# Performance work log

Measured on AMD Instinct MI355X. Metric: run time of the kernel, lower is better.

Reference implementation:

```python
import jax, jax.numpy as jnp
import numpy as np
import math

N, E, D, H, C, G = 100000, 1600000, 256, 256, 4, 512
LN_EPS = 1e-5


def _pe(n, d):
    # sinusoidal positional encoding, rows = node index
    pos = jnp.arange(n, dtype=jnp.float32)[:, None]                      # [n,1]
    div = jnp.exp(jnp.arange(0, d, 2, dtype=jnp.float32) * (-math.log(10000.0) / d))  # [d/2]
    ang = pos * div                                                      # [n,d/2]
    return jnp.stack([jnp.sin(ang), jnp.cos(ang)], axis=-1).reshape(n, d)


def setup_inputs() -> dict:
    key = jax.random.key(0)
    ks = jax.random.split(key, 24)
    w = lambda k, shp: (jax.random.normal(k, shp, jnp.float32) * 0.05)
    inp = {
        "x": jax.random.normal(ks[0], (N, D), jnp.float32),
        "W_ft": w(ks[1], (D, H)), "b_ft": jnp.zeros((H,), jnp.float32),
        "ln_g": jnp.ones((H,), jnp.float32), "ln_b": jnp.zeros((H,), jnp.float32),
        "W_g0": w(ks[2], (H, H)), "b_g0": jnp.zeros((H,), jnp.float32),
        "W_g1": w(ks[3], (H, H)), "b_g1": jnp.zeros((H,), jnp.float32),
        "W_g2": w(ks[4], (H, H)), "b_g2": jnp.zeros((H,), jnp.float32),
        "W_c0": w(ks[5], (H, H)), "b_c0": jnp.zeros((H,), jnp.float32),
        "W_c1": w(ks[6], (H, H // 2)), "b_c1": jnp.zeros((H // 2,), jnp.float32),
        "W_c2": w(ks[7], (H // 2, C)), "b_c2": jnp.zeros((C,), jnp.float32),
        "edge_index": jax.random.randint(ks[8], (2, E), 0, N, dtype=jnp.int32),
        "batch": jnp.sort(jax.random.randint(ks[9], (N,), 0, G, dtype=jnp.int32)),
    }
    return inp


def reference(x, W_ft, b_ft, ln_g, ln_b, W_g0, b_g0, W_g1, b_g1, W_g2, b_g2,
              W_c0, b_c0, W_c1, b_c1, W_c2, b_c2, edge_index, batch):
    # feature transform: Linear + ReLU + Dropout(eval) + LayerNorm
    h = jax.nn.relu(x @ W_ft + b_ft)
    mu = jnp.mean(h, axis=-1, keepdims=True)
    var = jnp.mean(jnp.square(h - mu), axis=-1, keepdims=True)
    h = (h - mu) * jax.lax.rsqrt(var + LN_EPS) * ln_g + ln_b
    # temporal positional encoding (intended per-node add)
    h = h + _pe(N, H)
    # GCN layers (PyG GCNConv: self-loops + symmetric degree norm + scatter-add)
    loops = jnp.arange(N, dtype=edge_index.dtype)
    src = jnp.concatenate([edge_index[0], loops])
    dst = jnp.concatenate([edge_index[1], loops])
    deg = jax.ops.segment_sum(jnp.ones_like(dst, dtype=h.dtype), dst, num_segments=N)
    dinv = jnp.where(deg > 0, jax.lax.rsqrt(jnp.maximum(deg, 1.0)), 0.0)
    norm = (dinv[src] * dinv[dst])[:, None]                              # [E+N,1]
    for W, b in ((W_g0, b_g0), (W_g1, b_g1), (W_g2, b_g2)):
        m = (h @ W)[src] * norm                                          # gather + scale
        h = jax.nn.relu(jax.ops.segment_sum(m, dst, num_segments=N) + b)
    # global mean pool per graph
    sums = jax.ops.segment_sum(h, batch, num_segments=G)
    cnts = jax.ops.segment_sum(jnp.ones((N,), h.dtype), batch, num_segments=G)
    pooled = sums / jnp.maximum(cnts, 1.0)[:, None]                      # [G,H]
    # classifier MLP
    z = jax.nn.relu(pooled @ W_c0 + b_c0)
    z = jax.nn.relu(z @ W_c1 + b_c1)
    return z @ W_c2 + b_c2                                               # [G,C]
```

## Files before the change

kernel.cpp:

```cpp
#include <hip/hip_runtime.h>
#include <math.h>


typedef __attribute__((ext_vector_type(8))) _Float16 half8;
typedef __attribute__((ext_vector_type(4))) float floatx4;
typedef __attribute__((ext_vector_type(8))) unsigned short us8;

union HU { _Float16 h; unsigned short u; };

static __device__ __forceinline__ unsigned short f2h(float f) {
    HU x; x.h = (_Float16)f; return x.u;
}
static __device__ __forceinline__ float h2f(unsigned short s) {
    HU x; x.u = s; return (float)x.h;
}

static __device__ __forceinline__ void gl_lds16(const void* g, void* l) {
    __builtin_amdgcn_global_load_lds(
        (const __attribute__((address_space(1))) unsigned int*)(g),
        (__attribute__((address_space(3))) unsigned int*)(l), 16, 0, 0);
}

static __device__ __forceinline__ float cw_trig(float ang, bool is_cos) {
    const float i2pi = 0.15915494309189535f;
    const float k = rintf(ang * i2pi);
    float r = fmaf(k, -6.28125f, ang);
    r = fmaf(k, -1.9352436065673828e-3f, r);
    r = fmaf(k, -6.3573019e-8f, r);
    const float rv = r * i2pi;
    return is_cos ? __builtin_amdgcn_cosf(rv) : __builtin_amdgcn_sinf(rv);
}

__global__ void tg_splitB(const float* __restrict__ W0, const float* __restrict__ W1,
                          const float* __restrict__ W2, const float* __restrict__ W3,
                          unsigned short* __restrict__ B0, unsigned short* __restrict__ B1,
                          unsigned short* __restrict__ B2, unsigned short* __restrict__ B3)
{
    const float* Ws[4] = {W0, W1, W2, W3};
    unsigned short* Bs[4] = {B0, B1, B2, B3};
    const float* W = Ws[blockIdx.z];
    unsigned short* Bt = Bs[blockIdx.z];

    __shared__ float T[64][68];
    const int tk = blockIdx.x * 64, tn = blockIdx.y * 64;
    const int t = threadIdx.x;
#pragma unroll
    for (int j = 0; j < 4; ++j) {
        const int idx = t + 256 * j;
        const int k = idx >> 4, c4 = (idx & 15) * 4;
        const float4 v = *(const float4*)&W[(size_t)(tk + k) * 256 + tn + c4];
        T[k][c4] = v.x; T[k][c4 + 1] = v.y; T[k][c4 + 2] = v.z; T[k][c4 + 3] = v.w;
    }
    __syncthreads();
#pragma unroll
    for (int j = 0; j < 4; ++j) {
        const int idx = t + 256 * j;
        const int n = idx >> 4, q = (idx & 15) * 4;
        unsigned short hh[4], ll[4];
#pragma unroll
        for (int i = 0; i < 4; ++i) {
            const float f = T[q + i][n];
            hh[i] = f2h(f);
            ll[i] = f2h(f - h2f(hh[i]));
        }
        uint2 hp, lp;
        hp.x = (unsigned)hh[0] | ((unsigned)hh[1] << 16);
        hp.y = (unsigned)hh[2] | ((unsigned)hh[3] << 16);
        lp.x = (unsigned)ll[0] | ((unsigned)ll[1] << 16);
        lp.y = (unsigned)ll[2] | ((unsigned)ll[3] << 16);
        unsigned short* row = Bt + (size_t)(tn + n) * 512;
        *(uint2*)&row[tk + q]       = hp;
        *(uint2*)&row[256 + tk + q] = lp;
    }
}

__global__ __launch_bounds__(256, 2)
void tg_ft_ln(const float* __restrict__ x, const unsigned short* __restrict__ Bt,
              const float* __restrict__ bias, const float* __restrict__ lng,
              const float* __restrict__ lnb, unsigned short* __restrict__ hh, int N)
{
    __shared__ unsigned short sAh[128 * 64];
    __shared__ unsigned short sAl[128 * 64];
    __shared__ unsigned short sB[256 * 64];
    __shared__ float sStats[128][2][2];
    __shared__ float sDiv[128];

    const int t = threadIdx.x;
    const int w = t >> 6, lane = t & 63;
    const int quad = lane >> 4, l16 = lane & 15;
    const int wr = w >> 1, wc = w & 1;
    const int row0 = blockIdx.x * 128;

    if (t < 128) sDiv[t] = expf((float)(2 * t) * -0.035977892078031970f);

    floatx4 acc[4][8];
#pragma unroll
    for (int i = 0; i < 4; ++i)
#pragma unroll
        for (int j = 0; j < 8; ++j) acc[i][j] = (floatx4){0.f, 0.f, 0.f, 0.f};

    const int arow = t >> 1;
    const int ahalf = t & 1;
    const int srow = lane >> 3;
    const int kgx  = (lane & 7) ^ srow;
    const int rsw  = l16 & 7;

    for (int k4 = 0; k4 < 4; ++k4) {
        const int ka = k4 * 64;
        if (k4) __syncthreads();
#pragma unroll
        for (int i = 0; i < 8; ++i) {
            const int rr = w * 64 + i * 8;
            gl_lds16(Bt + (size_t)(rr + srow) * 512 + ka + kgx * 8, &sB[rr * 64]);
        }
        {
            const int grow = row0 + arow;
            const bool ok = grow < N;
            const float* xp = x + (size_t)grow * 256 + ka + ahalf * 32;
#pragma unroll
            for (int j = 0; j < 4; ++j) {
                const int kg = ahalf * 4 + j;
                float4 v0 = {0.f, 0.f, 0.f, 0.f}, v1 = {0.f, 0.f, 0.f, 0.f};
                if (ok) {
                    v0 = *(const float4*)(xp + j * 8);
                    v1 = *(const float4*)(xp + j * 8 + 4);
                }
                const float f[8] = {v0.x, v0.y, v0.z, v0.w, v1.x, v1.y, v1.z, v1.w};
                us8 hi, lo;
#pragma unroll
                for (int i = 0; i < 8; ++i) {
                    hi[i] = f2h(f[i]);
                    lo[i] = f2h(f[i] - h2f(hi[i]));
                }
                const int ad = arow * 64 + ((kg ^ (arow & 7)) << 3);
                *(us8*)&sAh[ad] = hi;
                *(us8*)&sAl[ad] = lo;
            }
        }
        __syncthreads();
#pragma unroll
        for (int ks = 0; ks < 2; ++ks) {
            const int kq = ks * 4 + quad;
            half8 afh[4], afl[4];
#pragma unroll
            for (int rt = 0; rt < 4; ++rt) {
                const int r = wr * 64 + rt * 16 + l16;
                const int off = r * 64 + ((kq ^ rsw) << 3);
                afh[rt] = *(const half8*)&sAh[off];
                afl[rt] = *(const half8*)&sAl[off];
            }
#pragma unroll
            for (int cb = 0; cb < 2; ++cb) {
                half8 bfr[4];
#pragma unroll
                for (int c4 = 0; c4 < 4; ++c4) {
                    const int n = wc * 128 + (cb * 4 + c4) * 16 + l16;
                    bfr[c4] = *(const half8*)&sB[n * 64 + ((kq ^ rsw) << 3)];
                }
#pragma unroll
                for (int c4 = 0; c4 < 4; ++c4)
#pragma unroll
                    for (int rt = 0; rt < 4; ++rt) {
                        acc[rt][cb * 4 + c4] = __builtin_amdgcn_mfma_f32_16x16x32_f16(
                            afh[rt], bfr[c4], acc[rt][cb * 4 + c4], 0, 0, 0);
                        acc[rt][cb * 4 + c4] = __builtin_amdgcn_mfma_f32_16x16x32_f16(
                            afl[rt], bfr[c4], acc[rt][cb * 4 + c4], 0, 0, 0);
                    }
            }
        }
        __syncthreads();
#pragma unroll
        for (int i = 0; i < 8; ++i) {
            const int rr = w * 64 + i * 8;
            gl_lds16(Bt + (size_t)(rr + srow) * 512 + 256 + ka + kgx * 8, &sB[rr * 64]);
        }
        __syncthreads();
#pragma unroll
        for (int ks = 0; ks < 2; ++ks) {
            const int kq = ks * 4 + quad;
            half8 afh[4];
#pragma unroll
            for (int rt = 0; rt < 4; ++rt) {
                const int r = wr * 64 + rt * 16 + l16;
                afh[rt] = *(const half8*)&sAh[r * 64 + ((kq ^ rsw) << 3)];
            }
#pragma unroll
            for (int cb = 0; cb < 2; ++cb) {
                half8 bfr[4];
#pragma unroll
                for (int c4 = 0; c4 < 4; ++c4) {
                    const int n = wc * 128 + (cb * 4 + c4) * 16 + l16;
                    bfr[c4] = *(const half8*)&sB[n * 64 + ((kq ^ rsw) << 3)];
                }
#pragma unroll
                for (int c4 = 0; c4 < 4; ++c4)
#pragma unroll
                    for (int rt = 0; rt < 4; ++rt)
                        acc[rt][cb * 4 + c4] = __builtin_amdgcn_mfma_f32_16x16x32_f16(
                            afh[rt], bfr[c4], acc[rt][cb * 4 + c4], 0, 0, 0);
            }
        }
    }

    float bs[8], gs[8], bv[8], dv[8];
#pragma unroll
    for (int ct = 0; ct < 8; ++ct) {
        const int gc = wc * 128 + ct * 16 + l16;
        bs[ct] = bias[gc]; gs[ct] = lng[gc]; bv[ct] = lnb[gc];
        dv[ct] = sDiv[gc >> 1];
    }

#pragma unroll
    for (int rt = 0; rt < 4; ++rt) {
#pragma unroll
        for (int i = 0; i < 4; ++i) {
            float s = 0.f, q = 0.f;
#pragma unroll
            for (int ct = 0; ct < 8; ++ct) {
                const float v = fmaxf(acc[rt][ct][i] + bs[ct], 0.f);
                s += v; q += v * v;
            }
#pragma unroll
            for (int m = 1; m < 16; m <<= 1) {
                s += __shfl_xor(s, m, 64);
                q += __shfl_xor(q, m, 64);
            }
            if (l16 == 0) {
                const int rl = wr * 64 + rt * 16 + quad * 4 + i;
                sStats[rl][wc][0] = s;
                sStats[rl][wc][1] = q;
            }
        }
    }
    __syncthreads();

    const bool is_cos = (l16 & 1);
#pragma unroll
    for (int rt = 0; rt < 4; ++rt) {
#pragma unroll
        for (int i = 0; i < 4; ++i) {
            const int rl = wr * 64 + rt * 16 + quad * 4 + i;
            const int gr = row0 + rl;
            if (gr >= N) continue;
            const float sum = sStats[rl][0][0] + sStats[rl][1][0];
            const float sq  = sStats[rl][0][1] + sStats[rl][1][1];
            const float mu  = sum * (1.f / 256.f);
            const float var = sq * (1.f / 256.f) - mu * mu;
            const float rstd = 1.f / sqrtf(var + 1e-5f);
            const float rf = (float)gr;
            unsigned short* orow = hh + (size_t)gr * 256 + wc * 128 + l16;
#pragma unroll
            for (int ct = 0; ct < 8; ++ct) {
                const float v = fmaxf(acc[rt][ct][i] + bs[ct], 0.f);
                const float nrm = (v - mu) * rstd * gs[ct] + bv[ct];
                const float pe = cw_trig(rf * dv[ct], is_cos);
                orow[ct * 16] = f2h(nrm + pe);
            }
        }
    }
}

__global__ __launch_bounds__(256, 3)
void tg_gemm(const unsigned short* __restrict__ Ph,
             const unsigned short* __restrict__ Bt,
             const float* __restrict__ rowscale,
             unsigned short* __restrict__ out)
{
    __shared__ unsigned short sA[128 * 64], sB[128 * 64];

    const int t = threadIdx.x;
    const int w = t >> 6, lane = t & 63;
    const int quad = lane >> 4, l16 = lane & 15;
    const int wr = w >> 1, wc = w & 1;

    const int nwg = gridDim.x;
    const int swq = nwg >> 3, swr = nwg & 7;
    const int xcd = blockIdx.x & 7, oidx = blockIdx.x >> 3;
    const int lg = (xcd < swr ? xcd * (swq + 1)
                              : swr * (swq + 1) + (xcd - swr) * swq) + oidx;
    const int row0 = (lg >> 1) * 128;
    const int col0 = (lg & 1) * 128;

    floatx4 acc[4][4];
#pragma unroll
    for (int i = 0; i < 4; ++i)
#pragma unroll
        for (int j = 0; j < 4; ++j) acc[i][j] = (floatx4){0.f, 0.f, 0.f, 0.f};

    const int srow = lane >> 3;
    const int kgx  = (lane & 7) ^ srow;
    const int rsw  = l16 & 7;

    for (int c = 0; c < 8; ++c) {
        const int ka = (c >> 1) << 6;
        const int kb = ((c & 1) << 8) + ka;
        const bool stA = !(c & 1);
        if (c) __syncthreads();
#pragma unroll
        for (int i = 0; i < 4; ++i) {
            const int rr = w * 32 + i * 8;
            if (stA)
                gl_lds16(Ph + (size_t)(row0 + rr + srow) * 256 + ka + kgx * 8, &sA[rr * 64]);
            gl_lds16(Bt + (size_t)(col0 + rr + srow) * 512 + kb + kgx * 8, &sB[rr * 64]);
        }
        __syncthreads();
#pragma unroll
        for (int ks = 0; ks < 2; ++ks) {
            const int kq = ks * 4 + quad;
            half8 af[4], bfr[4];
#pragma unroll
            for (int rt = 0; rt < 4; ++rt) {
                const int r = wr * 64 + rt * 16 + l16;
                af[rt] = *(const half8*)&sA[r * 64 + ((kq ^ rsw) << 3)];
            }
#pragma unroll
            for (int ct = 0; ct < 4; ++ct) {
                const int n = wc * 64 + ct * 16 + l16;
                bfr[ct] = *(const half8*)&sB[n * 64 + ((kq ^ rsw) << 3)];
            }
#pragma unroll
            for (int ct = 0; ct < 4; ++ct)
#pragma unroll
                for (int rt = 0; rt < 4; ++rt)
                    acc[rt][ct] = __builtin_amdgcn_mfma_f32_16x16x32_f16(
                        af[rt], bfr[ct], acc[rt][ct], 0, 0, 0);
        }
    }

#pragma unroll
    for (int rt = 0; rt < 4; ++rt) {
#pragma unroll
        for (int i = 0; i < 4; ++i) {
            const int gr = row0 + wr * 64 + rt * 16 + quad * 4 + i;
            const float s = rowscale[gr];
#pragma unroll
            for (int ct = 0; ct < 4; ++ct) {
                const int gc = col0 + wc * 64 + ct * 16 + l16;
                out[(size_t)gr * 256 + gc] = f2h(acc[rt][ct][i] * s);
            }
        }
    }
}

__global__ void tg_count(const int* __restrict__ dst, int* __restrict__ deg,
                         int* __restrict__ perm, int E)
{
    const int e = blockIdx.x * blockDim.x + threadIdx.x;
    if (e < E) perm[e] = atomicAdd(&deg[dst[e]], 1);
}

__global__ void tg_dinv(const int* __restrict__ deg, float* __restrict__ dinv, int N)
{
    const int i = blockIdx.x * blockDim.x + threadIdx.x;
    if (i < N) dinv[i] = 1.f / sqrtf((float)(deg[i] + 1));
}

__global__ void tg_scan1(const int* __restrict__ cnt, int* __restrict__ out,
                         int* __restrict__ sums, int N)
{
    __shared__ int tmp[1024];
    const int t = threadIdx.x;
    const int gid = blockIdx.x * 1024 + t;
    const int v = (gid < N) ? cnt[gid] : 0;
    tmp[t] = v;
    __syncthreads();
    for (int o = 1; o < 1024; o <<= 1) {
        const int add = (t >= o) ? tmp[t - o] : 0;
        __syncthreads();
        tmp[t] += add;
        __syncthreads();
    }
    if (gid < N) out[gid] = tmp[t] - v;
    if (t == 1023) sums[blockIdx.x] = tmp[t];
}

__global__ void tg_scan2(int* __restrict__ sums, int nb)
{
    __shared__ int tmp[1024];
    const int t = threadIdx.x;
    const int v = (t < nb) ? sums[t] : 0;
    tmp[t] = v;
    __syncthreads();
    for (int o = 1; o < 1024; o <<= 1) {
        const int add = (t >= o) ? tmp[t - o] : 0;
        __syncthreads();
        tmp[t] += add;
        __syncthreads();
    }
    if (t < nb) sums[t] = tmp[t] - v;
}

__global__ void tg_scan3(int* __restrict__ rowptr, const int* __restrict__ offs,
                         int N, int E)
{
    const int gid = blockIdx.x * 1024 + threadIdx.x;
    if (gid < N) rowptr[gid] += offs[gid >> 10];
    else if (gid == N) rowptr[N] = E;
}

__global__ void tg_fill(const int* __restrict__ src, const int* __restrict__ dst,
                        const int* __restrict__ rowptr, const int* __restrict__ perm,
                        int* __restrict__ col, int E)
{
    const int e = blockIdx.x * blockDim.x + threadIdx.x;
    if (e >= E) return;
    col[rowptr[dst[e]] + perm[e]] = src[e];
}

__global__ void tg_aggregate_h(const unsigned short* __restrict__ hwpb,
                               const int* __restrict__ rowptr, const int* __restrict__ col,
                               const float* __restrict__ dinv, const float* __restrict__ bias,
                               unsigned short* __restrict__ hh, int N)
{
    const int gt = blockIdx.x * blockDim.x + threadIdx.x;
    const int row = gt >> 5;
    if (row >= N) return;
    const int hl = gt & 31;
    const int c = hl * 8;

    const unsigned short* base = hwpb + c;
    const int beg = rowptr[row], end = rowptr[row + 1];

    const us8 sv = *(const us8*)(base + (size_t)row * 256);
    float a[8];
#pragma unroll
    for (int j = 0; j < 8; ++j) a[j] = h2f(sv[j]);

    int p = beg;
    int rem = end - beg;
    int c0[8];
    if (rem >= 8) {
#pragma unroll
        for (int u = 0; u < 8; ++u) c0[u] = col[p + u];
    }
    while (rem >= 8) {
        int c1[8];
        const bool more = rem >= 16;
        if (more) {
#pragma unroll
            for (int u = 0; u < 8; ++u) c1[u] = col[p + 8 + u];
        }
        us8 v[8];
#pragma unroll
        for (int u = 0; u < 8; ++u)
            v[u] = *(const us8*)(base + (size_t)c0[u] * 256);
#pragma unroll
        for (int u = 0; u < 8; ++u)
#pragma unroll
            for (int j = 0; j < 8; ++j) a[j] += h2f(v[u][j]);
        if (more) {
#pragma unroll
            for (int u = 0; u < 8; ++u) c0[u] = c1[u];
        }
        p += 8; rem -= 8;
    }
    if (rem > 0) {
        const int last = end - 1;
        int ci[8];
#pragma unroll
        for (int u = 0; u < 8; ++u) {
            const int pp = (p + u < last) ? p + u : last;
            ci[u] = col[pp];
        }
        us8 v[8];
#pragma unroll
        for (int u = 0; u < 8; ++u)
            v[u] = *(const us8*)(base + (size_t)(u < rem ? ci[u] : row) * 256);
#pragma unroll
        for (int u = 0; u < 8; ++u) {
            if (u < rem) {
#pragma unroll
                for (int j = 0; j < 8; ++j) a[j] += h2f(v[u][j]);
            }
        }
    }

    const float di = dinv[row];
    const float4 b0 = *(const float4*)&bias[c];
    const float4 b1 = *(const float4*)&bias[c + 4];
    us8 o;
    o[0] = f2h(fmaxf(di * a[0] + b0.x, 0.f));
    o[1] = f2h(fmaxf(di * a[1] + b0.y, 0.f));
    o[2] = f2h(fmaxf(di * a[2] + b0.z, 0.f));
    o[3] = f2h(fmaxf(di * a[3] + b0.w, 0.f));
    o[4] = f2h(fmaxf(di * a[4] + b1.x, 0.f));
    o[5] = f2h(fmaxf(di * a[5] + b1.y, 0.f));
    o[6] = f2h(fmaxf(di * a[6] + b1.z, 0.f));
    o[7] = f2h(fmaxf(di * a[7] + b1.w, 0.f));
    *(us8*)&hh[(size_t)row * 256 + c] = o;
}

__global__ void tg_ranges(const int* __restrict__ batch, int* __restrict__ starts,
                          int N, int G)
{
    const int g = blockIdx.x * blockDim.x + threadIdx.x;
    if (g > G) return;
    int lo = 0, hi = N;
    while (lo < hi) {
        const int mid = (lo + hi) >> 1;
        if (batch[mid] < g) lo = mid + 1; else hi = mid;
    }
    starts[g] = lo;
}

__global__ void tg_pool(const unsigned short* __restrict__ hh,
                        const int* __restrict__ starts, float* __restrict__ pooled, int G)
{
    __shared__ float sh[4][64][4];
    const int g = blockIdx.x;
    const int t = threadIdx.x;
    const int wv = t >> 6, lane = t & 63;
    const int c = lane * 4;
    const int beg = starts[g], end = starts[g + 1];
    float s0 = 0.f, s1 = 0.f, s2 = 0.f, s3 = 0.f;
    for (int r = beg + wv; r < end; r += 4) {
        const ushort4 vh = *(const ushort4*)&hh[(size_t)r * 256 + c];
        s0 += h2f(vh.x); s1 += h2f(vh.y); s2 += h2f(vh.z); s3 += h2f(vh.w);
    }
    sh[wv][lane][0] = s0; sh[wv][lane][1] = s1;
    sh[wv][lane][2] = s2; sh[wv][lane][3] = s3;
    __syncthreads();
    if (t < 64) {
        const float inv = 1.f / fmaxf((float)(end - beg), 1.f);
        float4 o;
        o.x = (sh[0][t][0] + sh[1][t][0] + sh[2][t][0] + sh[3][t][0]) * inv;
        o.y = (sh[0][t][1] + sh[1][t][1] + sh[2][t][1] + sh[3][t][1]) * inv;
        o.z = (sh[0][t][2] + sh[1][t][2] + sh[2][t][2] + sh[3][t][2]) * inv;
        o.w = (sh[0][t][3] + sh[1][t][3] + sh[2][t][3] + sh[3][t][3]) * inv;
        *(float4*)&pooled[(size_t)g * 256 + t * 4] = o;
    }
}

__global__ void tg_mlp(const float* __restrict__ A, const float* __restrict__ B,
                       const float* __restrict__ bias, float* __restrict__ Cout,
                       int M, int K, int Nc, int do_relu)
{
    const int idx = blockIdx.x * blockDim.x + threadIdx.x;
    if (idx >= M * Nc) return;
    const int m = idx / Nc;
    const int n = idx - m * Nc;
    float acc = 0.f;
    for (int k = 0; k < K; ++k) acc += A[(size_t)m * K + k] * B[(size_t)k * Nc + n];
    acc += bias[n];
    Cout[idx] = do_relu ? fmaxf(acc, 0.f) : acc;
}

extern "C" void kernel_launch(void* const* d_in, const int* in_sizes, int n_in,
                              void* d_out, int out_size, void* d_ws, size_t ws_size,
                              hipStream_t stream)
{
    const float* x    = (const float*)d_in[0];
    const float* W_ft = (const float*)d_in[1];
    const float* b_ft = (const float*)d_in[2];
    const float* ln_g = (const float*)d_in[3];
    const float* ln_b = (const float*)d_in[4];
    const float* W_g[3] = {(const float*)d_in[5], (const float*)d_in[7], (const float*)d_in[9]};
    const float* b_g[3] = {(const float*)d_in[6], (const float*)d_in[8], (const float*)d_in[10]};
    const float* W_c0 = (const float*)d_in[11];
    const float* b_c0 = (const float*)d_in[12];
    const float* W_c1 = (const float*)d_in[13];
    const float* b_c1 = (const float*)d_in[14];
    const float* W_c2 = (const float*)d_in[15];
    const float* b_c2 = (const float*)d_in[16];
    const int*   edge  = (const int*)d_in[17];
    const int*   batch = (const int*)d_in[18];

    const int N    = in_sizes[18];
    const int E    = in_sizes[17] / 2;
    const int Mpad = (N + 127) & ~127;
    const int H2   = in_sizes[14];
    const int Cc   = in_sizes[15] / H2;
    const int G    = out_size / Cc;

    const int* srcI = edge;
    const int* dstI = edge + E;

    size_t off = 0;
    auto alloc = [&](size_t bytes) {
        char* p = (char*)d_ws + off;
        off = (off + bytes + 255) & ~(size_t)255;
        return p;
    };
    unsigned short* hh   = (unsigned short*)alloc((size_t)Mpad * 256 * 2);
    unsigned short* hwpb = (unsigned short*)alloc((size_t)Mpad * 256 * 2);
    float* dinv   = (float*)alloc((size_t)Mpad * 4);
    int*   deg    = (int*)alloc((size_t)Mpad * 4);
    int*   rowptr = (int*)alloc((size_t)(N + 1) * 4);
    int*   perm   = (int*)alloc((size_t)E * 4);
    int*   col    = (int*)alloc((size_t)E * 4);
    int*   bsums  = (int*)alloc(1024 * 4);
    int*   starts = (int*)alloc((size_t)(G + 1) * 4);
    float* pooled = (float*)alloc((size_t)G * 256 * 4);
    float* z0     = (float*)alloc((size_t)G * 256 * 4);
    float* z1     = (float*)alloc((size_t)G * H2 * 4);
    unsigned short* Bt[4];
    for (int i = 0; i < 4; ++i)
        Bt[i] = (unsigned short*)alloc((size_t)256 * 512 * 2);
    (void)ws_size; (void)n_in;

    hipMemsetAsync(deg, 0, (size_t)Mpad * 4, stream);
    hipMemsetAsync(hh + (size_t)N * 256, 0, (size_t)(Mpad - N) * 256 * 2, stream);

    tg_splitB<<<dim3(4, 4, 4), dim3(256), 0, stream>>>(
        W_ft, W_g[0], W_g[1], W_g[2], Bt[0], Bt[1], Bt[2], Bt[3]);

    tg_ft_ln<<<dim3(Mpad / 128), dim3(256), 0, stream>>>(
        x, Bt[0], b_ft, ln_g, ln_b, hh, N);

    tg_count<<<dim3((E + 255) / 256), dim3(256), 0, stream>>>(dstI, deg, perm, E);
    tg_dinv<<<dim3((Mpad + 255) / 256), dim3(256), 0, stream>>>(deg, dinv, Mpad);
    const int NB = (N + 1023) / 1024;
    tg_scan1<<<dim3(NB), dim3(1024), 0, stream>>>(deg, rowptr, bsums, N);
    tg_scan2<<<dim3(1), dim3(1024), 0, stream>>>(bsums, NB);
    tg_scan3<<<dim3((N + 1024) / 1024), dim3(1024), 0, stream>>>(rowptr, bsums, N, E);
    tg_fill<<<dim3((E + 255) / 256), dim3(256), 0, stream>>>(srcI, dstI, rowptr, perm, col, E);

    const int nbx = (Mpad / 128) * 2;
    for (int l = 0; l < 3; ++l) {
        tg_gemm<<<dim3(nbx), dim3(256), 0, stream>>>(hh, Bt[l + 1], dinv, hwpb);
        tg_aggregate_h<<<dim3((N + 7) / 8), dim3(256), 0, stream>>>(hwpb, rowptr, col, dinv,
                                                                    b_g[l], hh, N);
    }

    tg_ranges<<<dim3((G + 256) / 256), dim3(256), 0, stream>>>(batch, starts, N, G);
    tg_pool<<<dim3(G), dim3(256), 0, stream>>>(hh, starts, pooled, G);

    tg_mlp<<<dim3((G * 256 + 255) / 256), dim3(256), 0, stream>>>(pooled, W_c0, b_c0, z0, G, 256, 256, 1);
    tg_mlp<<<dim3((G * H2 + 255) / 256), dim3(256), 0, stream>>>(z0, W_c1, b_c1, z1, G, 256, H2, 1);
    tg_mlp<<<dim3((G * Cc + 255) / 256), dim3(256), 0, stream>>>(z1, W_c2, b_c2, (float*)d_out, G, H2, Cc, 0);
}
```

Baseline: 1.061 ms.

## Merge edge count and fill into GEMM launches, fuse pooling ranges and MLP

Degree counting now runs as extra blocks of the feature-transform/LayerNorm launch, and CSR column filling runs as extra blocks of the first GCN GEMM launch, so these independent tasks overlap with compute-heavy work. Graph range search moves into the pool kernel, and the three classifier layers become one kernel per graph, which removes several small launches. Ping-pong P/Q buffers replace reusing hh within the layer loop, which costs an extra memset. The fused kernels carry the larger kernel's LDS footprint and launch bounds even for the lightweight atomic blocks.

```diff
diff --git a/kernel.cpp b/kernel.cpp
--- a/kernel.cpp
+++ b/kernel.cpp
@@ -75,17 +75,29 @@
 }
 
 __global__ __launch_bounds__(256, 2)
-void tg_ft_ln(const float* __restrict__ x, const unsigned short* __restrict__ Bt,
-              const float* __restrict__ bias, const float* __restrict__ lng,
-              const float* __restrict__ lnb, unsigned short* __restrict__ hh, int N)
-{
+void tg_ftln_count(const float* __restrict__ x, const unsigned short* __restrict__ Bt,
+                   const float* __restrict__ bias, const float* __restrict__ lng,
+                   const float* __restrict__ lnb, unsigned short* __restrict__ hh,
+                   int N, const int* __restrict__ dst, int* __restrict__ deg,
+                   int* __restrict__ perm, int E, int nft)
+{
+    const int t = threadIdx.x;
+    if ((int)blockIdx.x >= nft) {
+        const int base = ((int)blockIdx.x - nft) * 2048;
+#pragma unroll
+        for (int j = 0; j < 8; ++j) {
+            const int e = base + j * 256 + t;
+            if (e < E) perm[e] = atomicAdd(&deg[dst[e]], 1);
+        }
+        return;
+    }
+
     __shared__ unsigned short sAh[128 * 64];
     __shared__ unsigned short sAl[128 * 64];
     __shared__ unsigned short sB[256 * 64];
     __shared__ float sStats[128][2][2];
     __shared__ float sDiv[128];
 
-    const int t = threadIdx.x;
     const int w = t >> 6, lane = t & 63;
     const int quad = lane >> 4, l16 = lane & 15;
     const int wr = w >> 1, wc = w & 1;
@@ -260,93 +272,116 @@
     }
 }
 
+static __device__ __forceinline__
+void gemm_body(const unsigned short* __restrict__ Ph,
+               const unsigned short* __restrict__ Bt,
+               const float* __restrict__ rowscale,
+               unsigned short* __restrict__ out, int bid, int nwg)
+{
+    __shared__ unsigned short sA[128 * 64], sB[128 * 64];
+
+    const int t = threadIdx.x;
+    const int w = t >> 6, lane = t & 63;
+    const int quad = lane >> 4, l16 = lane & 15;
+    const int wr = w >> 1, wc = w & 1;
+
+    const int swq = nwg >> 3, swr = nwg & 7;
+    const int xcd = bid & 7, oidx = bid >> 3;
+    const int lg = (xcd < swr ? xcd * (swq + 1)
+                              : swr * (swq + 1) + (xcd - swr) * swq) + oidx;
+    const int row0 = (lg >> 1) * 128;
+    const int col0 = (lg & 1) * 128;
+
+    floatx4 acc[4][4];
+#pragma unroll
+    for (int i = 0; i < 4; ++i)
+#pragma unroll
+        for (int j = 0; j < 4; ++j) acc[i][j] = (floatx4){0.f, 0.f, 0.f, 0.f};
+
+    const int srow = lane >> 3;
+    const int kgx  = (lane & 7) ^ srow;
+    const int rsw  = l16 & 7;
+
+    for (int c = 0; c < 8; ++c) {
+        const int ka = (c >> 1) << 6;
+        const int kb = ((c & 1) << 8) + ka;
+        const bool stA = !(c & 1);
+        if (c) __syncthreads();
+#pragma unroll
+        for (int i = 0; i < 4; ++i) {
+            const int rr = w * 32 + i * 8;
+            if (stA)
+                gl_lds16(Ph + (size_t)(row0 + rr + srow) * 256 + ka + kgx * 8, &sA[rr * 64]);
+            gl_lds16(Bt + (size_t)(col0 + rr + srow) * 512 + kb + kgx * 8, &sB[rr * 64]);
+        }
+        __syncthreads();
+#pragma unroll
+        for (int ks = 0; ks < 2; ++ks) {
+            const int kq = ks * 4 + quad;
+            half8 af[4], bfr[4];
+#pragma unroll
+            for (int rt = 0; rt < 4; ++rt) {
+                const int r = wr * 64 + rt * 16 + l16;
+                af[rt] = *(const half8*)&sA[r * 64 + ((kq ^ rsw) << 3)];
+            }
+#pragma unroll
+            for (int ct = 0; ct < 4; ++ct) {
+                const int n = wc * 64 + ct * 16 + l16;
+                bfr[ct] = *(const half8*)&sB[n * 64 + ((kq ^ rsw) << 3)];
+            }
+#pragma unroll
+            for (int ct = 0; ct < 4; ++ct)
+#pragma unroll
+                for (int rt = 0; rt < 4; ++rt)
+                    acc[rt][ct] = __builtin_amdgcn_mfma_f32_16x16x32_f16(
+                        af[rt], bfr[ct], acc[rt][ct], 0, 0, 0);
+        }
+    }
+
+#pragma unroll
+    for (int rt = 0; rt < 4; ++rt) {
+#pragma unroll
+        for (int i = 0; i < 4; ++i) {
+            const int gr = row0 + wr * 64 + rt * 16 + quad * 4 + i;
+            const float s = rowscale[gr];
+#pragma unroll
+            for (int ct = 0; ct < 4; ++ct) {
+                const int gc = col0 + wc * 64 + ct * 16 + l16;
+                out[(size_t)gr * 256 + gc] = f2h(acc[rt][ct][i] * s);
+            }
+        }
+    }
+}
+
 __global__ __launch_bounds__(256, 3)
 void tg_gemm(const unsigned short* __restrict__ Ph,
              const unsigned short* __restrict__ Bt,
              const float* __restrict__ rowscale,
              unsigned short* __restrict__ out)
 {
-    __shared__ unsigned short sA[128 * 64], sB[128 * 64];
-
-    const int t = threadIdx.x;
-    const int w = t >> 6, lane = t & 63;
-    const int quad = lane >> 4, l16 = lane & 15;
-    const int wr = w >> 1, wc = w & 1;
-
-    const int nwg = gridDim.x;
-    const int swq = nwg >> 3, swr = nwg & 7;
-    const int xcd = blockIdx.x & 7, oidx = blockIdx.x >> 3;
-    const int lg = (xcd < swr ? xcd * (swq + 1)
-                              : swr * (swq + 1) + (xcd - swr) * swq) + oidx;
-    const int row0 = (lg >> 1) * 128;
-    const int col0 = (lg & 1) * 128;
-
-    floatx4 acc[4][4];
-#pragma unroll
-    for (int i = 0; i < 4; ++i)
-#pragma unroll
-        for (int j = 0; j < 4; ++j) acc[i][j] = (floatx4){0.f, 0.f, 0.f, 0.f};
-
-    const int srow = lane >> 3;
-    const int kgx  = (lane & 7) ^ srow;
-    const int rsw  = l16 & 7;
-
-    for (int c = 0; c < 8; ++c) {
-        const int ka = (c >> 1) << 6;
-        const int kb = ((c & 1) << 8) + ka;
-        const bool stA = !(c & 1);
-        if (c) __syncthreads();
-#pragma unroll
-        for (int i = 0; i < 4; ++i) {
-            const int rr = w * 32 + i * 8;
-            if (stA)
-                gl_lds16(Ph + (size_t)(row0 + rr + srow) * 256 + ka + kgx * 8, &sA[rr * 64]);
-            gl_lds16(Bt + (size_t)(col0 + rr + srow) * 512 + kb + kgx * 8, &sB[rr * 64]);
-        }
-        __syncthreads();
-#pragma unroll
-        for (int ks = 0; ks < 2; ++ks) {
-            const int kq = ks * 4 + quad;
-            half8 af[4], bfr[4];
-#pragma unroll
-            for (int rt = 0; rt < 4; ++rt) {
-                const int r = wr * 64 + rt * 16 + l16;
-                af[rt] = *(const half8*)&sA[r * 64 + ((kq ^ rsw) << 3)];
-            }
-#pragma unroll
-            for (int ct = 0; ct < 4; ++ct) {
-                const int n = wc * 64 + ct * 16 + l16;
-                bfr[ct] = *(const half8*)&sB[n * 64 + ((kq ^ rsw) << 3)];
-            }
-#pragma unroll
-            for (int ct = 0; ct < 4; ++ct)
-#pragma unroll
-                for (int rt = 0; rt < 4; ++rt)
-                    acc[rt][ct] = __builtin_amdgcn_mfma_f32_16x16x32_f16(
-                        af[rt], bfr[ct], acc[rt][ct], 0, 0, 0);
-        }
-    }
-
-#pragma unroll
-    for (int rt = 0; rt < 4; ++rt) {
-#pragma unroll
-        for (int i = 0; i < 4; ++i) {
-            const int gr = row0 + wr * 64 + rt * 16 + quad * 4 + i;
-            const float s = rowscale[gr];
-#pragma unroll
-            for (int ct = 0; ct < 4; ++ct) {
-                const int gc = col0 + wc * 64 + ct * 16 + l16;
-                out[(size_t)gr * 256 + gc] = f2h(acc[rt][ct][i] * s);
-            }
-        }
-    }
-}
-
-__global__ void tg_count(const int* __restrict__ dst, int* __restrict__ deg,
-                         int* __restrict__ perm, int E)
-{
-    const int e = blockIdx.x * blockDim.x + threadIdx.x;
-    if (e < E) perm[e] = atomicAdd(&deg[dst[e]], 1);
+    gemm_body(Ph, Bt, rowscale, out, (int)blockIdx.x, (int)gridDim.x);
+}
+
+__global__ __launch_bounds__(256, 3)
+void tg_gemm_fill(const unsigned short* __restrict__ Ph,
+                  const unsigned short* __restrict__ Bt,
+                  const float* __restrict__ rowscale,
+                  unsigned short* __restrict__ out,
+                  const int* __restrict__ src, const int* __restrict__ dst,
+                  const int* __restrict__ rowptr, const int* __restrict__ perm,
+                  int* __restrict__ col, int E, int nbx)
+{
+    const int t = threadIdx.x;
+    if ((int)blockIdx.x >= nbx) {
+        const int base = ((int)blockIdx.x - nbx) * 2048;
+#pragma unroll
+        for (int j = 0; j < 8; ++j) {
+            const int e = base + j * 256 + t;
+            if (e < E) col[rowptr[dst[e]] + perm[e]] = src[e];
+        }
+        return;
+    }
+    gemm_body(Ph, Bt, rowscale, out, (int)blockIdx.x, nbx);
 }
 
 __global__ void tg_dinv(const int* __restrict__ deg, float* __restrict__ dinv, int N)
@@ -396,15 +431,6 @@
     const int gid = blockIdx.x * 1024 + threadIdx.x;
     if (gid < N) rowptr[gid] += offs[gid >> 10];
     else if (gid == N) rowptr[N] = E;
-}
-
-__global__ void tg_fill(const int* __restrict__ src, const int* __restrict__ dst,
-                        const int* __restrict__ rowptr, const int* __restrict__ perm,
-                        int* __restrict__ col, int E)
-{
-    const int e = blockIdx.x * blockDim.x + threadIdx.x;
-    if (e >= E) return;
-    col[rowptr[dst[e]] + perm[e]] = src[e];
 }
 
 __global__ void tg_aggregate_h(const unsigned short* __restrict__ hwpb,
@@ -490,28 +516,27 @@
     *(us8*)&hh[(size_t)row * 256 + c] = o;
 }
 
-__global__ void tg_ranges(const int* __restrict__ batch, int* __restrict__ starts,
-                          int N, int G)
-{
-    const int g = blockIdx.x * blockDim.x + threadIdx.x;
-    if (g > G) return;
-    int lo = 0, hi = N;
-    while (lo < hi) {
-        const int mid = (lo + hi) >> 1;
-        if (batch[mid] < g) lo = mid + 1; else hi = mid;
-    }
-    starts[g] = lo;
-}
-
 __global__ void tg_pool(const unsigned short* __restrict__ hh,
-                        const int* __restrict__ starts, float* __restrict__ pooled, int G)
+                        const int* __restrict__ batch, float* __restrict__ pooled,
+                        int N, int G)
 {
     __shared__ float sh[4][64][4];
+    __shared__ int sBE[2];
     const int g = blockIdx.x;
     const int t = threadIdx.x;
+    if (t < 2) {
+        const int target = g + t;
+        int lo = 0, hi = N;
+        while (lo < hi) {
+            const int mid = (lo + hi) >> 1;
+            if (batch[mid] < target) lo = mid + 1; else hi = mid;
+        }
+        sBE[t] = lo;
+    }
+    __syncthreads();
+    const int beg = sBE[0], end = sBE[1];
     const int wv = t >> 6, lane = t & 63;
     const int c = lane * 4;
-    const int beg = starts[g], end = starts[g + 1];
     float s0 = 0.f, s1 = 0.f, s2 = 0.f, s3 = 0.f;
     for (int r = beg + wv; r < end; r += 4) {
         const ushort4 vh = *(const ushort4*)&hh[(size_t)r * 256 + c];
@@ -531,18 +556,35 @@
     }
 }
 
-__global__ void tg_mlp(const float* __restrict__ A, const float* __restrict__ B,
-                       const float* __restrict__ bias, float* __restrict__ Cout,
-                       int M, int K, int Nc, int do_relu)
-{
-    const int idx = blockIdx.x * blockDim.x + threadIdx.x;
-    if (idx >= M * Nc) return;
-    const int m = idx / Nc;
-    const int n = idx - m * Nc;
-    float acc = 0.f;
-    for (int k = 0; k < K; ++k) acc += A[(size_t)m * K + k] * B[(size_t)k * Nc + n];
-    acc += bias[n];
-    Cout[idx] = do_relu ? fmaxf(acc, 0.f) : acc;
+__global__ __launch_bounds__(256)
+void tg_mlp3(const float* __restrict__ pooled,
+             const float* __restrict__ W0, const float* __restrict__ b0,
+             const float* __restrict__ W1, const float* __restrict__ b1,
+             const float* __restrict__ W2, const float* __restrict__ b2,
+             float* __restrict__ out, int H2, int Cc)
+{
+    __shared__ float zin[256];
+    __shared__ float z0[256];
+    __shared__ float z1[256];
+    const int g = blockIdx.x;
+    const int t = threadIdx.x;
+    zin[t] = pooled[(size_t)g * 256 + t];
+    __syncthreads();
+    float a = 0.f;
+    for (int k = 0; k < 256; ++k) a += zin[k] * W0[(size_t)k * 256 + t];
+    z0[t] = fmaxf(a + b0[t], 0.f);
+    __syncthreads();
+    if (t < H2) {
+        float a1 = 0.f;
+        for (int k = 0; k < 256; ++k) a1 += z0[k] * W1[(size_t)k * H2 + t];
+        z1[t] = fmaxf(a1 + b1[t], 0.f);
+    }
+    __syncthreads();
+    if (t < Cc) {
+        float a2 = 0.f;
+        for (int k = 0; k < H2; ++k) a2 += z1[k] * W2[(size_t)k * Cc + t];
+        out[(size_t)g * Cc + t] = a2 + b2[t];
+    }
 }
 
 extern "C" void kernel_launch(void* const* d_in, const int* in_sizes, int n_in,
@@ -581,18 +623,16 @@
         off = (off + bytes + 255) & ~(size_t)255;
         return p;
     };
-    unsigned short* hh   = (unsigned short*)alloc((size_t)Mpad * 256 * 2);
-    unsigned short* hwpb = (unsigned short*)alloc((size_t)Mpad * 256 * 2);
+    unsigned short* hh  = (unsigned short*)alloc((size_t)Mpad * 256 * 2);
+    unsigned short* P   = (unsigned short*)alloc((size_t)Mpad * 256 * 2);
+    unsigned short* Q   = (unsigned short*)alloc((size_t)Mpad * 256 * 2);
     float* dinv   = (float*)alloc((size_t)Mpad * 4);
     int*   deg    = (int*)alloc((size_t)Mpad * 4);
     int*   rowptr = (int*)alloc((size_t)(N + 1) * 4);
     int*   perm   = (int*)alloc((size_t)E * 4);
     int*   col    = (int*)alloc((size_t)E * 4);
     int*   bsums  = (int*)alloc(1024 * 4);
-    int*   starts = (int*)alloc((size_t)(G + 1) * 4);
     float* pooled = (float*)alloc((size_t)G * 256 * 4);
-    float* z0     = (float*)alloc((size_t)G * 256 * 4);
-    float* z1     = (float*)alloc((size_t)G * H2 * 4);
     unsigned short* Bt[4];
     for (int i = 0; i < 4; ++i)
         Bt[i] = (unsigned short*)alloc((size_t)256 * 512 * 2);
@@ -600,32 +640,37 @@
 
     hipMemsetAsync(deg, 0, (size_t)Mpad * 4, stream);
     hipMemsetAsync(hh + (size_t)N * 256, 0, (size_t)(Mpad - N) * 256 * 2, stream);
+    hipMemsetAsync(Q + (size_t)N * 256, 0, (size_t)(Mpad - N) * 256 * 2, stream);
 
     tg_splitB<<<dim3(4, 4, 4), dim3(256), 0, stream>>>(
         W_ft, W_g[0], W_g[1], W_g[2], Bt[0], Bt[1], Bt[2], Bt[3]);
 
-    tg_ft_ln<<<dim3(Mpad / 128), dim3(256), 0, stream>>>(
-        x, Bt[0], b_ft, ln_g, ln_b, hh, N);
-
-    tg_count<<<dim3((E + 255) / 256), dim3(256), 0, stream>>>(dstI, deg, perm, E);
+    const int nft  = Mpad / 128;
+    const int ncnt = (E + 2047) / 2048;
+    tg_ftln_count<<<dim3(nft + ncnt), dim3(256), 0, stream>>>(
+        x, Bt[0], b_ft, ln_g, ln_b, hh, N, dstI, deg, perm, E, nft);
+
     tg_dinv<<<dim3((Mpad + 255) / 256), dim3(256), 0, stream>>>(deg, dinv, Mpad);
     const int NB = (N + 1023) / 1024;
     tg_scan1<<<dim3(NB), dim3(1024), 0, stream>>>(deg, rowptr, bsums, N);
     tg_scan2<<<dim3(1), dim3(1024), 0, stream>>>(bsums, NB);
     tg_scan3<<<dim3((N + 1024) / 1024), dim3(1024), 0, stream>>>(rowptr, bsums, N, E);
-    tg_fill<<<dim3((E + 255) / 256), dim3(256), 0, stream>>>(srcI, dstI, rowptr, perm, col, E);
 
     const int nbx = (Mpad / 128) * 2;
-    for (int l = 0; l < 3; ++l) {
-        tg_gemm<<<dim3(nbx), dim3(256), 0, stream>>>(hh, Bt[l + 1], dinv, hwpb);
-        tg_aggregate_h<<<dim3((N + 7) / 8), dim3(256), 0, stream>>>(hwpb, rowptr, col, dinv,
-                                                                    b_g[l], hh, N);
-    }
-
-    tg_ranges<<<dim3((G + 256) / 256), dim3(256), 0, stream>>>(batch, starts, N, G);
-    tg_pool<<<dim3(G), dim3(256), 0, stream>>>(hh, starts, pooled, G);
-
-    tg_mlp<<<dim3((G * 256 + 255) / 256), dim3(256), 0, stream>>>(pooled, W_c0, b_c0, z0, G, 256, 256, 1);
-    tg_mlp<<<dim3((G * H2 + 255) / 256), dim3(256), 0, stream>>>(z0, W_c1, b_c1, z1, G, 256, H2, 1);
-    tg_mlp<<<dim3((G * Cc + 255) / 256), dim3(256), 0, stream>>>(z1, W_c2, b_c2, (float*)d_out, G, H2, Cc, 0);
-}
+    const int nfl = (E + 2047) / 2048;
+    tg_gemm_fill<<<dim3(nbx + nfl), dim3(256), 0, stream>>>(
+        hh, Bt[1], dinv, P, srcI, dstI, rowptr, perm, col, E, nbx);
+    tg_aggregate_h<<<dim3((N + 7) / 8), dim3(256), 0, stream>>>(P, rowptr, col, dinv,
+                                                                b_g[0], Q, N);
+    tg_gemm<<<dim3(nbx), dim3(256), 0, stream>>>(Q, Bt[2], dinv, P);
+    tg_aggregate_h<<<dim3((N + 7) / 8), dim3(256), 0, stream>>>(P, rowptr, col, dinv,
+                                                                b_g[1], Q, N);
+    tg_gemm<<<dim3(nbx), dim3(256), 0, stream>>>(Q, Bt[3], dinv, P);
+    tg_aggregate_h<<<dim3((N + 7) / 8), dim3(256), 0, stream>>>(P, rowptr, col, dinv,
+                                                                b_g[2], hh, N);
+
+    tg_pool<<<dim3(G), dim3(256), 0, stream>>>(hh, batch, pooled, N, G);
+
+    tg_mlp3<<<dim3(G), dim3(256), 0, stream>>>(pooled, W_c0, b_c0, W_c1, b_c1,
+                                               W_c2, b_c2, (float*)d_out, H2, Cc);
+}
```

After: 873.9 us. -17.7%, faster.
